# Kernel tuning notes

Hardware: AMD Instinct MI355X
Metric: run time of the kernel (lower is better)

## Reference

```python
import jax, jax.numpy as jnp
import numpy as np

GRID_SIZE = 5
SPLINE_ORDER = 3
GRID_RANGE = (-1.0, 1.0)
IN_FEATURES = 1024
OUT_FEATURES = 1024
NUM_BASIS = GRID_SIZE + SPLINE_ORDER  # 8
SCALE_BASE = 1.0
SCALE_SPLINE = 1.0

_h = (GRID_RANGE[1] - GRID_RANGE[0]) / GRID_SIZE
_GRID = np.linspace(GRID_RANGE[0] - SPLINE_ORDER * _h,
                    GRID_RANGE[1] + SPLINE_ORDER * _h,
                    GRID_SIZE + 2 * SPLINE_ORDER + 1).astype(np.float32)  # (12,)


def bspline_basis(x, grid):
    # x: (B, I)  ->  basis: (B, I, NUM_BASIS)
    x = jnp.clip(x, GRID_RANGE[0], GRID_RANGE[1])
    xg = x[..., None]                              # (B, I, 1)
    g = grid                                       # (G,) broadcasts over (B, I)
    basis = ((xg >= g[:-1]) & (xg < g[1:])).astype(x.dtype)  # (B, I, G-1)
    for k in range(1, SPLINE_ORDER + 1):
        left_den = g[k:-1] - g[:-(k + 1)]
        left_den = jnp.where(left_den == 0, jnp.ones_like(left_den), left_den)
        right_den = g[k + 1:] - g[1:-k]
        right_den = jnp.where(right_den == 0, jnp.ones_like(right_den), right_den)
        left = (xg - g[:-(k + 1)]) / left_den * basis[..., :-1]
        right = (g[k + 1:] - xg) / right_den * basis[..., 1:]
        basis = left + right
    return basis


def setup_inputs() -> dict:
    key = jax.random.key(0)
    k1, k2, k3 = jax.random.split(key, 3)
    x = jax.random.normal(k1, (8192, IN_FEATURES), dtype=jnp.float32)
    base_weight = jax.random.normal(k2, (OUT_FEATURES, IN_FEATURES), dtype=jnp.float32) * 0.03
    spline_weight = jax.random.normal(k3, (OUT_FEATURES, IN_FEATURES, NUM_BASIS), dtype=jnp.float32) * 0.03
    return {"x": x, "base_weight": base_weight, "spline_weight": spline_weight}


def reference(x, base_weight, spline_weight):
    grid = jnp.asarray(_GRID, dtype=x.dtype)
    # base branch: SiLU(x) @ W_base^T
    base_out = jax.nn.silu(x) @ base_weight.T              # (B, O)
    base_out = base_out * SCALE_BASE
    # spline branch: einsum over (in, basis)
    basis = bspline_basis(x, grid)                         # (B, I, K)
    spline_out = jnp.einsum('bik,oik->bo', basis, spline_weight)
    spline_out = spline_out * SCALE_SPLINE
    return base_out + spline_out
```

## Files before the change

### kernel.cpp

```cpp
#include <hip/hip_runtime.h>
#include <hip/hip_bf16.h>
#include <cstdint>


typedef short s16x8 __attribute__((ext_vector_type(8)));
typedef float f32x4 __attribute__((ext_vector_type(4)));

#define GK 9216
#define GN 1024
#define GI 1024
#define GM 8192

#define BK 32
#define NT 288

#define BS_BLK 32768
#define RP_BLK 4608

__device__ __forceinline__ void cp16(const __hip_bfloat16* g, __hip_bfloat16* l) {
  __builtin_amdgcn_global_load_lds((const __attribute__((address_space(1))) void*)g,
                                   (__attribute__((address_space(3))) void*)l, 16, 0, 0);
}

__device__ __forceinline__ uint32_t bfbits(float f) {
  __hip_bfloat16 h = __float2bfloat16(f);
  unsigned short us;
  __builtin_memcpy(&us, &h, 2);
  return (uint32_t)us;
}

__device__ __forceinline__ void basis4(float xv, int& jj, float& w0, float& w1,
                                       float& w2, float& w3) {
  float t = fminf(1.f, fmaxf(-1.f, xv));
  float us = (t + 1.f) * 2.5f;
  int j = (int)us;
  if (j > 4) j = 4;
  float u = us - (float)j;
  float u2 = u * u, u3 = u2 * u;
  float om = 1.f - u;
  jj = j;
  w0 = om * om * om * (1.f / 6.f);
  w1 = (3.f * u3 - 6.f * u2 + 4.f) * (1.f / 6.f);
  w2 = (-3.f * u3 + 3.f * u2 + 3.f * u + 1.f) * (1.f / 6.f);
  w3 = u3 * (1.f / 6.f);
}

__global__ void kan_prep_all(const float* __restrict__ x,
                             const float* __restrict__ baseW,
                             const float* __restrict__ splineW,
                             __hip_bfloat16* __restrict__ W2,
                             __hip_bfloat16* __restrict__ A) {
  int bid = blockIdx.x;
  if (bid < BS_BLK) {
    int t = bid * 256 + threadIdx.x;
    int b = t >> 10, i = t & 1023;
    float xv = x[t];

    float sl = xv / (1.f + __expf(-xv));
    A[(size_t)b * GK + 8192 + i] = __float2bfloat16(sl);

    int jj; float w0, w1, w2, w3;
    basis4(xv, jj, w0, w1, w2, w3);
    uint64_t W64 = (uint64_t)(bfbits(w0) | (bfbits(w1) << 16)) |
                   ((uint64_t)(bfbits(w2) | (bfbits(w3) << 16)) << 32);
    int sh = jj * 16;
    uint64_t lo = (jj < 4) ? (W64 << sh) : 0ull;
    uint64_t hi = (jj == 0) ? 0ull : (W64 >> (64 - sh));
    uint4 pk;
    pk.x = (uint32_t)lo;  pk.y = (uint32_t)(lo >> 32);
    pk.z = (uint32_t)hi;  pk.w = (uint32_t)(hi >> 32);
    *(uint4*)(A + (size_t)b * GK + (size_t)i * 8) = pk;
  } else {
    int t = (bid - BS_BLK) * 256 + threadIdx.x;
    int o = t / 1152;
    int c = (t - o * 1152) * 8;
    const float* src = (c < 8192) ? (splineW + (size_t)o * 8192 + c)
                                  : (baseW + (size_t)o * GI + (c - 8192));
    float4 v0 = ((const float4*)src)[0];
    float4 v1 = ((const float4*)src)[1];
    uint4 pk;
    pk.x = bfbits(v0.x) | (bfbits(v0.y) << 16);
    pk.y = bfbits(v0.z) | (bfbits(v0.w) << 16);
    pk.z = bfbits(v1.x) | (bfbits(v1.y) << 16);
    pk.w = bfbits(v1.z) | (bfbits(v1.w) << 16);
    *(uint4*)(W2 + (size_t)o * GK + c) = pk;
  }
}

__global__ __launch_bounds__(512, 4) void kan_gemm_bc(
    const __hip_bfloat16* __restrict__ A,
    const __hip_bfloat16* __restrict__ B,
    float* __restrict__ C) {
  __shared__ __align__(16) __hip_bfloat16 As[3][128 * BK];
  __shared__ __align__(16) __hip_bfloat16 Bs[3][256 * BK];
  const int tid = threadIdx.x;
  const int lane = tid & 63;
  const int wave = tid >> 6;
  const int wm = wave >> 2, wn = wave & 3;

  const int linear = blockIdx.y * 4 + blockIdx.x;
  const int c = (linear & 7) * 32 + (linear >> 3);
  const int colBand = c & 3;
  const int rowBand = c >> 2;
  const int blockRow = rowBand * 128;
  const int blockCol = colBand * 256;

  const int srow = tid >> 2;
  const int sq = tid & 3;
  const int ssw = sq ^ ((srow >> 1) & 3);
  const __hip_bfloat16* aSrc = A + (size_t)(blockRow + srow) * GK + ssw * 8;
  const __hip_bfloat16* bSrc = B + (size_t)(blockCol + srow) * GK + ssw * 8;
  const int ldsOff = wave * 512;

#define STAGE(T, BUF)                                             \
  do {                                                            \
    const __hip_bfloat16* ga = aSrc + (T) * BK;                   \
    const __hip_bfloat16* gb = bSrc + (T) * BK;                   \
    cp16(ga, As[BUF] + ldsOff);                                   \
    cp16(gb, Bs[BUF] + ldsOff);                                   \
    cp16(gb + 128 * GK, Bs[BUF] + ldsOff + 4096);                 \
  } while (0)

  const int q = lane >> 4, r16 = lane & 15;
  const int qs = q ^ ((r16 >> 1) & 3);
  const int aBase = (wm * 64 + r16) * 4 + qs;
  const int bBase = (wn * 64 + r16) * 4 + qs;

  f32x4 acc[4][4] = {};

  STAGE(0, 0);
  __builtin_amdgcn_sched_barrier(0);
  STAGE(1, 1);
  __builtin_amdgcn_sched_barrier(0);
  STAGE(2, 2);
  __builtin_amdgcn_sched_barrier(0);
  asm volatile("s_waitcnt vmcnt(6)" ::: "memory");
  __builtin_amdgcn_sched_barrier(0);
  __builtin_amdgcn_s_barrier();

  for (int t3 = 0; t3 < NT / 3; ++t3) {
#pragma unroll
    for (int u = 0; u < 3; ++u) {
      const int t = t3 * 3 + u;
      const int tp = (t + 3 < NT) ? (t + 3) : 0;
      __builtin_amdgcn_sched_barrier(0);
      const s16x8* Af = (const s16x8*)As[u];
      const s16x8* Bf = (const s16x8*)Bs[u];
      s16x8 af[4], bfg[4];
#pragma unroll
      for (int tm = 0; tm < 4; ++tm) af[tm] = Af[aBase + tm * 64];
#pragma unroll
      for (int tn = 0; tn < 4; ++tn) bfg[tn] = Bf[bBase + tn * 64];
      asm volatile("s_waitcnt lgkmcnt(0)" ::: "memory");
      __builtin_amdgcn_sched_barrier(0);
      __builtin_amdgcn_s_barrier();
      __builtin_amdgcn_sched_barrier(0);
      STAGE(tp, u);
      __builtin_amdgcn_sched_barrier(0);
      __builtin_amdgcn_s_setprio(1);
#pragma unroll
      for (int tm = 0; tm < 4; ++tm)
#pragma unroll
        for (int tn = 0; tn < 4; ++tn)
          acc[tm][tn] = __builtin_amdgcn_mfma_f32_16x16x32_bf16(
              af[tm], bfg[tn], acc[tm][tn], 0, 0, 0);
      __builtin_amdgcn_s_setprio(0);
      asm volatile("s_waitcnt vmcnt(6)" ::: "memory");
      __builtin_amdgcn_sched_barrier(0);
      __builtin_amdgcn_s_barrier();
    }
  }
  asm volatile("s_waitcnt vmcnt(0)" ::: "memory");

  const int cRow0 = blockRow + wm * 64 + q * 4;
  const int cCol0 = blockCol + wn * 64 + r16;
#pragma unroll
  for (int tm = 0; tm < 4; ++tm)
#pragma unroll
    for (int tn = 0; tn < 4; ++tn) {
      int col = cCol0 + tn * 16;
      size_t base = (size_t)(cRow0 + tm * 16) * GN + col;
#pragma unroll
      for (int r = 0; r < 4; ++r)
        C[base + (size_t)r * GN] = acc[tm][tn][r];
    }
#undef STAGE
}

__global__ void kan_naive(const float* __restrict__ x,
                          const float* __restrict__ bw,
                          const float* __restrict__ sw,
                          float* __restrict__ out) {
  int o = blockIdx.x * 256 + threadIdx.x;
  int b = blockIdx.y;
  float acc = 0.f;
  for (int i = 0; i < GI; ++i) {
    float xv = x[(size_t)b * GI + i];
    float sl = xv / (1.f + __expf(-xv));
    acc += sl * bw[(size_t)o * GI + i];
    int jj; float w0, w1, w2, w3;
    basis4(xv, jj, w0, w1, w2, w3);
    const float* swr = sw + ((size_t)o * GI + i) * 8 + jj;
    acc += w0 * swr[0] + w1 * swr[1] + w2 * swr[2] + w3 * swr[3];
  }
  out[(size_t)b * GN + o] = acc;
}

extern "C" void kernel_launch(void* const* d_in, const int* in_sizes, int n_in,
                              void* d_out, int out_size, void* d_ws, size_t ws_size,
                              hipStream_t stream) {
  const float* x  = (const float*)d_in[0];
  const float* bw = (const float*)d_in[1];
  const float* sw = (const float*)d_in[2];
  float* out = (float*)d_out;

  const size_t wBytes = (size_t)GK * GN * 2;
  const size_t aBytes = (size_t)GM * GK * 2;

  if (ws_size < wBytes + aBytes) {
    kan_naive<<<dim3(GN / 256, GM), 256, 0, stream>>>(x, bw, sw, out);
    return;
  }

  __hip_bfloat16* W2 = (__hip_bfloat16*)d_ws;
  __hip_bfloat16* Abuf = W2 + (size_t)GK * GN;

  kan_prep_all<<<BS_BLK + RP_BLK, 256, 0, stream>>>(x, bw, sw, W2, Abuf);
  kan_gemm_bc<<<dim3(4, 64), 512, 0, stream>>>(Abuf, W2, out);
}
```

Before: 315.6 us.

## Use 256x256 tiles with split-K of two and add partial-sum reduction

The GEMM moves from 128x256 tiles with BK=32 and triple buffering to 256x256 tiles with BK=64 and double buffering. The K dimension is split in two so the grid still has 256 blocks; each half writes to its own buffer, and a separate reduce kernel adds them. Inside the loop, LDS fragment loads and MFMA groups are interleaved with finer waits to overlap memory and compute. The cost is an extra 32MB partial buffer, an extra kernel launch with its read/write traffic, and lower occupancy (launch bounds go from 4 to 2).

```diff
diff --git a/kernel.cpp b/kernel.cpp
--- a/kernel.cpp
+++ b/kernel.cpp
@@ -11,11 +11,13 @@
 #define GI 1024
 #define GM 8192
 
-#define BK 32
-#define NT 288
+#define KSPLIT 4608
+#define NTK 72
 
 #define BS_BLK 32768
 #define RP_BLK 4608
+
+#define SB __builtin_amdgcn_sched_barrier(0)
 
 __device__ __forceinline__ void cp16(const __hip_bfloat16* g, __hip_bfloat16* l) {
   __builtin_amdgcn_global_load_lds((const __attribute__((address_space(1))) void*)g,
@@ -87,104 +89,139 @@
   }
 }
 
-__global__ __launch_bounds__(512, 4) void kan_gemm_bc(
+__global__ __launch_bounds__(512, 2) void kan_gemm_pl(
     const __hip_bfloat16* __restrict__ A,
     const __hip_bfloat16* __restrict__ B,
-    float* __restrict__ C) {
-  __shared__ __align__(16) __hip_bfloat16 As[3][128 * BK];
-  __shared__ __align__(16) __hip_bfloat16 Bs[3][256 * BK];
+    float* __restrict__ C0,
+    float* __restrict__ C1) {
+  __shared__ __align__(16) __hip_bfloat16 As[2][16384];
+  __shared__ __align__(16) __hip_bfloat16 Bs[2][16384];
   const int tid = threadIdx.x;
   const int lane = tid & 63;
   const int wave = tid >> 6;
   const int wm = wave >> 2, wn = wave & 3;
 
-  const int linear = blockIdx.y * 4 + blockIdx.x;
+  const int linear = blockIdx.x;
   const int c = (linear & 7) * 32 + (linear >> 3);
-  const int colBand = c & 3;
-  const int rowBand = c >> 2;
-  const int blockRow = rowBand * 128;
+  const int ks = c >> 7;
+  const int cc = c & 127;
+  const int colBand = cc & 3;
+  const int rowBand = cc >> 2;
+  const int blockRow = rowBand * 256;
   const int blockCol = colBand * 256;
-
-  const int srow = tid >> 2;
-  const int sq = tid & 3;
-  const int ssw = sq ^ ((srow >> 1) & 3);
-  const __hip_bfloat16* aSrc = A + (size_t)(blockRow + srow) * GK + ssw * 8;
-  const __hip_bfloat16* bSrc = B + (size_t)(blockCol + srow) * GK + ssw * 8;
-  const int ldsOff = wave * 512;
-
-#define STAGE(T, BUF)                                             \
-  do {                                                            \
-    const __hip_bfloat16* ga = aSrc + (T) * BK;                   \
-    const __hip_bfloat16* gb = bSrc + (T) * BK;                   \
-    cp16(ga, As[BUF] + ldsOff);                                   \
-    cp16(gb, Bs[BUF] + ldsOff);                                   \
-    cp16(gb + 128 * GK, Bs[BUF] + ldsOff + 4096);                 \
+  const int kbase = ks * KSPLIT;
+
+  const int srow8 = tid >> 3;
+  const int so = tid & 7;
+  const int ssw = so ^ (srow8 & 7);
+  const __hip_bfloat16* aSrc = A + (size_t)(blockRow + srow8) * GK + kbase + ssw * 8;
+  const __hip_bfloat16* bSrc = B + (size_t)(blockCol + srow8) * GK + kbase + ssw * 8;
+  const int ldsW = wave * 512;
+
+#define STAGE_AU(U, T, NB) cp16(aSrc + (size_t)(U) * 64 * GK + (size_t)(T) * 64, \
+                                As[NB] + (U) * 4096 + ldsW)
+#define STAGE_BU(U, T, NB) cp16(bSrc + (size_t)(U) * 64 * GK + (size_t)(T) * 64, \
+                                Bs[NB] + (U) * 4096 + ldsW)
+
+  const int q = lane >> 4, r16 = lane & 15;
+  const int swz = r16 & 7;
+  const int s0 = q ^ swz;
+  const int s1 = (4 + q) ^ swz;
+  const int aBase0 = (wm * 128 + r16) * 8 + s0;
+  const int aBase1 = (wm * 128 + r16) * 8 + s1;
+  const int bBase0 = (wn * 64 + r16) * 8 + s0;
+  const int bBase1 = (wn * 64 + r16) * 8 + s1;
+
+  f32x4 acc[8][4] = {};
+
+#define MPAIR(P, AR)                                                          \
+  do {                                                                        \
+    __builtin_amdgcn_s_setprio(1);                                            \
+    _Pragma("unroll")                                                         \
+    for (int n = 0; n < 4; ++n) {                                             \
+      acc[2*(P)][n]   = __builtin_amdgcn_mfma_f32_16x16x32_bf16(AR[0], b0[n], acc[2*(P)][n],   0, 0, 0); \
+      acc[2*(P)][n]   = __builtin_amdgcn_mfma_f32_16x16x32_bf16(AR[1], b1[n], acc[2*(P)][n],   0, 0, 0); \
+      acc[2*(P)+1][n] = __builtin_amdgcn_mfma_f32_16x16x32_bf16(AR[2], b0[n], acc[2*(P)+1][n], 0, 0, 0); \
+      acc[2*(P)+1][n] = __builtin_amdgcn_mfma_f32_16x16x32_bf16(AR[3], b1[n], acc[2*(P)+1][n], 0, 0, 0); \
+    }                                                                         \
+    __builtin_amdgcn_s_setprio(0);                                            \
   } while (0)
 
-  const int q = lane >> 4, r16 = lane & 15;
-  const int qs = q ^ ((r16 >> 1) & 3);
-  const int aBase = (wm * 64 + r16) * 4 + qs;
-  const int bBase = (wn * 64 + r16) * 4 + qs;
-
-  f32x4 acc[4][4] = {};
-
-  STAGE(0, 0);
-  __builtin_amdgcn_sched_barrier(0);
-  STAGE(1, 1);
-  __builtin_amdgcn_sched_barrier(0);
-  STAGE(2, 2);
-  __builtin_amdgcn_sched_barrier(0);
-  asm volatile("s_waitcnt vmcnt(6)" ::: "memory");
-  __builtin_amdgcn_sched_barrier(0);
+  STAGE_AU(0, 0, 0); STAGE_AU(1, 0, 0); STAGE_AU(2, 0, 0); STAGE_AU(3, 0, 0);
+  STAGE_BU(0, 0, 0); STAGE_BU(1, 0, 0); STAGE_BU(2, 0, 0); STAGE_BU(3, 0, 0);
+  asm volatile("s_waitcnt vmcnt(0)" ::: "memory");
+  SB;
   __builtin_amdgcn_s_barrier();
 
-  for (int t3 = 0; t3 < NT / 3; ++t3) {
-#pragma unroll
-    for (int u = 0; u < 3; ++u) {
-      const int t = t3 * 3 + u;
-      const int tp = (t + 3 < NT) ? (t + 3) : 0;
-      __builtin_amdgcn_sched_barrier(0);
-      const s16x8* Af = (const s16x8*)As[u];
-      const s16x8* Bf = (const s16x8*)Bs[u];
-      s16x8 af[4], bfg[4];
-#pragma unroll
-      for (int tm = 0; tm < 4; ++tm) af[tm] = Af[aBase + tm * 64];
-#pragma unroll
-      for (int tn = 0; tn < 4; ++tn) bfg[tn] = Bf[bBase + tn * 64];
-      asm volatile("s_waitcnt lgkmcnt(0)" ::: "memory");
-      __builtin_amdgcn_sched_barrier(0);
-      __builtin_amdgcn_s_barrier();
-      __builtin_amdgcn_sched_barrier(0);
-      STAGE(tp, u);
-      __builtin_amdgcn_sched_barrier(0);
-      __builtin_amdgcn_s_setprio(1);
-#pragma unroll
-      for (int tm = 0; tm < 4; ++tm)
-#pragma unroll
-        for (int tn = 0; tn < 4; ++tn)
-          acc[tm][tn] = __builtin_amdgcn_mfma_f32_16x16x32_bf16(
-              af[tm], bfg[tn], acc[tm][tn], 0, 0, 0);
-      __builtin_amdgcn_s_setprio(0);
-      asm volatile("s_waitcnt vmcnt(6)" ::: "memory");
-      __builtin_amdgcn_sched_barrier(0);
-      __builtin_amdgcn_s_barrier();
-    }
-  }
-  asm volatile("s_waitcnt vmcnt(0)" ::: "memory");
-
-  const int cRow0 = blockRow + wm * 64 + q * 4;
+  for (int t = 0; t < NTK; ++t) {
+    const int cb = t & 1, nb = cb ^ 1;
+    const int tp = (t + 1 < NTK) ? (t + 1) : 0;
+    const s16x8* Af = (const s16x8*)As[cb];
+    const s16x8* Bf = (const s16x8*)Bs[cb];
+    s16x8 b0[4], b1[4], aA[4], aB[4];
+
+#pragma unroll
+    for (int n = 0; n < 4; ++n) { b0[n] = Bf[bBase0 + n * 128]; b1[n] = Bf[bBase1 + n * 128]; }
+    aA[0] = Af[aBase0];        aA[1] = Af[aBase1];
+    aA[2] = Af[aBase0 + 128];  aA[3] = Af[aBase1 + 128];
+    SB;
+    aB[0] = Af[aBase0 + 256];  aB[1] = Af[aBase1 + 256];
+    aB[2] = Af[aBase0 + 384];  aB[3] = Af[aBase1 + 384];
+    SB;
+    STAGE_AU(0, tp, nb); STAGE_AU(1, tp, nb); STAGE_AU(2, tp, nb); STAGE_AU(3, tp, nb);
+    SB;
+    asm volatile("s_waitcnt lgkmcnt(4)" ::: "memory");
+    SB;
+    MPAIR(0, aA);
+    SB;
+    aA[0] = Af[aBase0 + 512];  aA[1] = Af[aBase1 + 512];
+    aA[2] = Af[aBase0 + 640];  aA[3] = Af[aBase1 + 640];
+    SB;
+    STAGE_BU(0, tp, nb); STAGE_BU(1, tp, nb); STAGE_BU(2, tp, nb); STAGE_BU(3, tp, nb);
+    SB;
+    asm volatile("s_waitcnt lgkmcnt(4)" ::: "memory");
+    SB;
+    MPAIR(1, aB);
+    SB;
+    aB[0] = Af[aBase0 + 768];  aB[1] = Af[aBase1 + 768];
+    aB[2] = Af[aBase0 + 896];  aB[3] = Af[aBase1 + 896];
+    SB;
+    asm volatile("s_waitcnt lgkmcnt(4)" ::: "memory");
+    SB;
+    MPAIR(2, aA);
+    SB;
+    asm volatile("s_waitcnt lgkmcnt(0)" ::: "memory");
+    SB;
+    MPAIR(3, aB);
+    asm volatile("s_waitcnt vmcnt(0)" ::: "memory");
+    SB;
+    __builtin_amdgcn_s_barrier();
+  }
+
+  float* __restrict__ Cd = ks ? C1 : C0;
+  const int cRow0 = blockRow + wm * 128 + q * 4;
   const int cCol0 = blockCol + wn * 64 + r16;
 #pragma unroll
-  for (int tm = 0; tm < 4; ++tm)
+  for (int tm = 0; tm < 8; ++tm)
 #pragma unroll
     for (int tn = 0; tn < 4; ++tn) {
       int col = cCol0 + tn * 16;
       size_t base = (size_t)(cRow0 + tm * 16) * GN + col;
 #pragma unroll
       for (int r = 0; r < 4; ++r)
-        C[base + (size_t)r * GN] = acc[tm][tn][r];
+        Cd[base + (size_t)r * GN] = acc[tm][tn][r];
     }
-#undef STAGE
+#undef MPAIR
+#undef STAGE_AU
+#undef STAGE_BU
+}
+
+__global__ void kan_reduce(float* __restrict__ out, const float* __restrict__ part) {
+  size_t i = ((size_t)blockIdx.x * 256 + threadIdx.x) * 4;
+  float4 a = *(const float4*)(out + i);
+  float4 b = *(const float4*)(part + i);
+  a.x += b.x; a.y += b.y; a.z += b.z; a.w += b.w;
+  *(float4*)(out + i) = a;
 }
 
 __global__ void kan_naive(const float* __restrict__ x,
@@ -216,15 +253,18 @@
 
   const size_t wBytes = (size_t)GK * GN * 2;
   const size_t aBytes = (size_t)GM * GK * 2;
-
-  if (ws_size < wBytes + aBytes) {
+  const size_t pBytes = (size_t)GM * GN * 4;
+
+  if (ws_size < wBytes + aBytes + pBytes) {
     kan_naive<<<dim3(GN / 256, GM), 256, 0, stream>>>(x, bw, sw, out);
     return;
   }
 
   __hip_bfloat16* W2 = (__hip_bfloat16*)d_ws;
   __hip_bfloat16* Abuf = W2 + (size_t)GK * GN;
+  float* partial = (float*)((char*)d_ws + wBytes + aBytes);
 
   kan_prep_all<<<BS_BLK + RP_BLK, 256, 0, stream>>>(x, bw, sw, W2, Abuf);
-  kan_gemm_bc<<<dim3(4, 64), 512, 0, stream>>>(Abuf, W2, out);
-}
+  kan_gemm_pl<<<dim3(256), 512, 0, stream>>>(Abuf, W2, out, partial);
+  kan_reduce<<<GM * GN / (256 * 4), 256, 0, stream>>>(out, partial);
+}
```

Measured after the change: 262.8 us. -16.7%, faster.
